# Optimization experiments

Measured on AMD Instinct MI355X. Metric: run time of the kernel, lower is better.

## Reference

```python
import jax, jax.numpy as jnp
import numpy as np

DIM = 1024
NUM_HEADS = 16
HEAD_DIM = DIM // NUM_HEADS
SCALE = HEAD_DIM ** -0.5


def setup_inputs() -> dict:
    key = jax.random.key(0)
    k1, k2, k3 = jax.random.split(key, 3)
    B, S = 2, 2048
    x = jax.random.normal(k1, (B, S, DIM), dtype=jnp.float32)
    # nn.Linear(dim, 3*dim, bias=False): store as [in, out] for x @ W
    w_qkv = jax.random.normal(k2, (DIM, 3 * DIM), dtype=jnp.float32) * (DIM ** -0.5)
    w_out = jax.random.normal(k3, (DIM, DIM), dtype=jnp.float32) * (DIM ** -0.5)
    return {"x": x, "w_qkv": w_qkv, "w_out": w_out}


def reference(x, w_qkv, w_out):
    B, S, _ = x.shape
    qkv = x @ w_qkv                               # [B,S,3*D]
    q, k, v = jnp.split(qkv, 3, axis=-1)          # each [B,S,D]
    def heads(t):
        return t.reshape(B, S, NUM_HEADS, HEAD_DIM).transpose(0, 2, 1, 3)  # [B,H,S,d]
    q, k, v = heads(q), heads(k), heads(v)
    scores = jnp.einsum('bhqd,bhkd->bhqk', q, k) * SCALE   # [B,H,S,S]
    probs = jax.nn.softmax(scores, axis=-1)
    out = jnp.einsum('bhqk,bhkd->bhqd', probs, v)          # [B,H,S,d]
    out = out.transpose(0, 2, 1, 3).reshape(B, S, DIM)
    return out @ w_out
```

## Files before the change

kernel.cpp:

```cpp
#include <hip/hip_runtime.h>


typedef __bf16 bf16x8 __attribute__((ext_vector_type(8)));
typedef __bf16 bf16x4 __attribute__((ext_vector_type(4)));
typedef float floatx4 __attribute__((ext_vector_type(4)));

#define MFMA16(a, b, c) __builtin_amdgcn_mfma_f32_16x16x32_bf16((a), (b), (c), 0, 0, 0)

__device__ __forceinline__ void gl_lds16(const void* g, void* l) {
  __builtin_amdgcn_global_load_lds((__attribute__((address_space(1))) void*)(g),
                                   (__attribute__((address_space(3))) void*)(l),
                                   16, 0, 0);
}

__global__ __launch_bounds__(256) void cast_x(const float* __restrict__ x,
                                              __bf16* __restrict__ xb) {
  int i = (blockIdx.x * 256 + threadIdx.x) * 4;
  float4 v = *(const float4*)(x + i);
  bf16x4 o = { (__bf16)v.x, (__bf16)v.y, (__bf16)v.z, (__bf16)v.w };
  *(bf16x4*)(xb + i) = o;
}

__global__ __launch_bounds__(256) void transpose_cast(const float* __restrict__ w,
                                                      __bf16* __restrict__ wt,
                                                      int K, int N) {
  __shared__ float tile[64][65];
  int k0 = blockIdx.x * 64, n0 = blockIdx.y * 64;
  int t = threadIdx.x;
  for (int j = 0; j < 16; ++j) {
    int e = j * 256 + t, r = e >> 6, c = e & 63;
    tile[r][c] = w[(size_t)(k0 + r) * N + n0 + c];
  }
  __syncthreads();
  for (int j = 0; j < 16; ++j) {
    int e = j * 256 + t, r = e >> 6, c = e & 63;
    wt[(size_t)(n0 + r) * K + k0 + c] = (__bf16)tile[c][r];
  }
}

template <typename OutT, bool SPLITV>
__global__ __launch_bounds__(256) void gemm_bt(const __bf16* __restrict__ A,
                                               const __bf16* __restrict__ Bt,
                                               OutT* __restrict__ C,
                                               __bf16* __restrict__ vt, int N) {
  constexpr int K = 1024;
  __shared__ __align__(16) __bf16 aS[128 * 32];
  __shared__ __align__(16) __bf16 bS[128 * 32];
  const int t = threadIdx.x;
  const int lane = t & 63, wave = t >> 6;
  const int l15 = lane & 15, quad = lane >> 4;
  const int wm = wave >> 1, wn = wave & 1;
  const int m0 = blockIdx.y * 128, n0 = blockIdx.x * 128;

  const floatx4 fzero = {0.f, 0.f, 0.f, 0.f};
  floatx4 acc[4][4];
  for (int mt = 0; mt < 4; ++mt)
    for (int nt = 0; nt < 4; ++nt) acc[mt][nt] = fzero;

  const int arow = t >> 2;
  const int ach = ((t & 3) ^ (arow & 3)) * 8;
  const __bf16* gA0 = A + (size_t)(m0 + arow) * K + ach;
  const __bf16* gA1 = gA0 + (size_t)64 * K;
  const __bf16* gB0 = Bt + (size_t)(n0 + arow) * K + ach;
  const __bf16* gB1 = gB0 + (size_t)64 * K;
  const int swz = (quad ^ (l15 & 3)) * 8;

  for (int k0 = 0; k0 < K; k0 += 32) {
    __syncthreads();
    gl_lds16(gA0 + k0, (char*)aS + t * 16);
    gl_lds16(gA1 + k0, (char*)aS + 4096 + t * 16);
    gl_lds16(gB0 + k0, (char*)bS + t * 16);
    gl_lds16(gB1 + k0, (char*)bS + 4096 + t * 16);
    __syncthreads();

    bf16x8 af[4], bfr[4];
    for (int mt = 0; mt < 4; ++mt)
      af[mt] = *(const bf16x8*)(aS + (wm * 64 + mt * 16 + l15) * 32 + swz);
    for (int nt = 0; nt < 4; ++nt)
      bfr[nt] = *(const bf16x8*)(bS + (wn * 64 + nt * 16 + l15) * 32 + swz);
    for (int mt = 0; mt < 4; ++mt)
      for (int nt = 0; nt < 4; ++nt)
        acc[mt][nt] = MFMA16(af[mt], bfr[nt], acc[mt][nt]);
  }

  for (int mt = 0; mt < 4; ++mt) {
    int row = m0 + wm * 64 + mt * 16 + quad * 4;
    for (int nt = 0; nt < 4; ++nt) {
      int col0 = n0 + wn * 64 + nt * 16;
      if (SPLITV && col0 >= 2048) {
        int dfull = col0 + l15 - 2048;
        int bh = ((row >> 11) << 4) + (dfull >> 6);
        int d = dfull & 63, s0 = row & 2047;
        bf16x4 pk = { (__bf16)acc[mt][nt][0], (__bf16)acc[mt][nt][1],
                      (__bf16)acc[mt][nt][2], (__bf16)acc[mt][nt][3] };
        *(bf16x4*)(vt + ((size_t)bh * 64 + d) * 2048 + s0) = pk;
      } else {
        int col = col0 + l15;
        OutT* cp = C + (size_t)row * N + col;
        for (int r = 0; r < 4; ++r) cp[(size_t)r * N] = (OutT)acc[mt][nt][r];
      }
    }
  }
}

__global__ __launch_bounds__(256) void flash_attn(const __bf16* __restrict__ qkv,
                                                  const __bf16* __restrict__ vt,
                                                  __bf16* __restrict__ out) {
  constexpr float SCALE = 0.125f;
  __shared__ __align__(16) __bf16 kS[2 * 64 * 64];
  __shared__ __align__(16) __bf16 vS[2 * 64 * 64];
  __shared__ __align__(16) __bf16 pT[64 * 64];

  const int t = threadIdx.x;
  const int lane = t & 63, wave = t >> 6;
  const int l15 = lane & 15, quad = lane >> 4;
  const int qb = blockIdx.x, bh = blockIdx.y;
  const int b = bh >> 4, h = bh & 15;

  bf16x8 qf[2][2];
  for (int qt = 0; qt < 2; ++qt) {
    const __bf16* qp = qkv +
        (size_t)(b * 2048 + qb * 128 + wave * 32 + qt * 16 + l15) * 3072 + h * 64 + quad * 8;
    qf[qt][0] = *(const bf16x8*)qp;
    qf[qt][1] = *(const bf16x8*)(qp + 32);
  }

  const floatx4 fzero = {0.f, 0.f, 0.f, 0.f};
  floatx4 oacc[2][4];
  float lsum[2] = {0.f, 0.f};
  for (int qt = 0; qt < 2; ++qt)
    for (int dt = 0; dt < 4; ++dt) oacc[qt][dt] = fzero;

  const int srow = t >> 3, schk = (t & 7) ^ (srow & 7);
  const __bf16* kg0 =
      qkv + (size_t)(b * 2048 + srow) * 3072 + 1024 + h * 64 + schk * 8;
  const __bf16* kg1 = kg0 + (size_t)32 * 3072;
  const __bf16* vg0 = vt + (size_t)bh * 64 * 2048 + (size_t)srow * 2048 + schk * 8;
  const __bf16* vg1 = vg0 + (size_t)32 * 2048;

  const int l7 = l15 & 7;
  const int prow = wave * 16 + l15;

  gl_lds16(kg0, (char*)kS + t * 16);
  gl_lds16(kg1, (char*)kS + 4096 + t * 16);
  gl_lds16(vg0, (char*)vS + t * 16);
  gl_lds16(vg1, (char*)vS + 4096 + t * 16);

  for (int nb = 0; nb < 32; ++nb) {
    __syncthreads();

    if (nb < 31) {
      const size_t n1 = (size_t)(nb + 1) * 64;
      const int oB = ((nb + 1) & 1) * 8192;
      gl_lds16(kg0 + n1 * 3072, (char*)kS + oB + t * 16);
      gl_lds16(kg1 + n1 * 3072, (char*)kS + oB + 4096 + t * 16);
      gl_lds16(vg0 + n1, (char*)vS + oB + t * 16);
      gl_lds16(vg1 + n1, (char*)vS + oB + 4096 + t * 16);
    }

    const __bf16* kC = kS + (nb & 1) * 4096;
    const __bf16* vC = vS + (nb & 1) * 4096;

    bf16x8 kf[4][2];
    for (int nt = 0; nt < 4; ++nt)
      for (int ks = 0; ks < 2; ++ks)
        kf[nt][ks] = *(const bf16x8*)(kC + (nt * 16 + l15) * 64 +
                                      ((ks * 4 + quad) ^ l7) * 8);
    bf16x8 vf[2][4];
    for (int ks = 0; ks < 2; ++ks)
      for (int dt = 0; dt < 4; ++dt)
        vf[ks][dt] = *(const bf16x8*)(vC + (dt * 16 + l15) * 64 +
                                      ((ks * 4 + quad) ^ l7) * 8);

    for (int qt = 0; qt < 2; ++qt) {
      floatx4 sa[4];
      for (int nt = 0; nt < 4; ++nt) {
        floatx4 a = fzero;
        a = MFMA16(kf[nt][0], qf[qt][0], a);
        a = MFMA16(kf[nt][1], qf[qt][1], a);
        sa[nt] = a;
      }
      float ls = 0.f;
      __bf16* pw = pT + (size_t)prow * 64;
      for (int nt = 0; nt < 4; ++nt) {
        float p0 = __expf(sa[nt][0] * SCALE);
        float p1 = __expf(sa[nt][1] * SCALE);
        float p2 = __expf(sa[nt][2] * SCALE);
        float p3 = __expf(sa[nt][3] * SCALE);
        ls += (p0 + p1) + (p2 + p3);
        bf16x4 pk = { (__bf16)p0, (__bf16)p1, (__bf16)p2, (__bf16)p3 };
        *(bf16x4*)(pw + ((nt * 2 + (quad >> 1)) ^ l7) * 8 + (quad & 1) * 4) = pk;
      }
      lsum[qt] += ls;
      for (int ks = 0; ks < 2; ++ks) {
        bf16x8 pa = *(const bf16x8*)(pw + ((ks * 4 + quad) ^ l7) * 8);
        for (int dt = 0; dt < 4; ++dt)
          oacc[qt][dt] = MFMA16(pa, vf[ks][dt], oacc[qt][dt]);
      }
    }
  }

  for (int qt = 0; qt < 2; ++qt) {
    float ls = lsum[qt];
    ls += __shfl_xor(ls, 16);
    ls += __shfl_xor(ls, 32);
    float inv[4];
    for (int r = 0; r < 4; ++r) inv[r] = 1.f / __shfl(ls, quad * 4 + r);
    __bf16* ob = out +
        (size_t)(b * 2048 + qb * 128 + wave * 32 + qt * 16 + quad * 4) * 1024 + h * 64;
    for (int dt = 0; dt < 4; ++dt)
      for (int r = 0; r < 4; ++r)
        ob[(size_t)r * 1024 + dt * 16 + l15] = (__bf16)(oacc[qt][dt][r] * inv[r]);
  }
}

extern "C" void kernel_launch(void* const* d_in, const int* in_sizes, int n_in,
                              void* d_out, int out_size, void* d_ws, size_t ws_size,
                              hipStream_t stream) {
  const float* x = (const float*)d_in[0];
  const float* w_qkv = (const float*)d_in[1];
  const float* w_out = (const float*)d_in[2];
  float* out = (float*)d_out;

  char* ws = (char*)d_ws;
  __bf16* xb = (__bf16*)(ws);
  __bf16* wqkvt = (__bf16*)(ws + ((size_t)8 << 20));
  __bf16* woutt = (__bf16*)(ws + ((size_t)14 << 20));
  __bf16* qkv = (__bf16*)(ws + ((size_t)16 << 20));
  __bf16* vtg = (__bf16*)(ws + ((size_t)40 << 20));
  __bf16* aout = (__bf16*)(ws + ((size_t)48 << 20));

  cast_x<<<4096, 256, 0, stream>>>(x, xb);
  transpose_cast<<<dim3(16, 48), 256, 0, stream>>>(w_qkv, wqkvt, 1024, 3072);
  transpose_cast<<<dim3(16, 16), 256, 0, stream>>>(w_out, woutt, 1024, 1024);
  gemm_bt<__bf16, true><<<dim3(24, 32), 256, 0, stream>>>(xb, wqkvt, qkv, vtg, 3072);
  flash_attn<<<dim3(16, 32), 256, 0, stream>>>(qkv, vtg, aout);
  gemm_bt<float, false><<<dim3(8, 32), 256, 0, stream>>>(aout, woutt, out, nullptr, 1024);
}
```

Measured before the change: 210.4 us.

## Fuse prep kernels, double query tile per attention block, add narrow-N output GEMM

Merges the x cast and both weight transpose-casts into one prep kernel, removing two launches. Flash attention now covers 256 queries per block (64 per wave), so each K/V tile loaded into LDS serves twice as many queries, at the cost of more registers, launch_bounds(256,1) and half as many blocks (256). The output projection uses a new 128x64-tile GEMM, giving 512 blocks instead of 256 to fill more CUs, with single-buffered K loop and syncs on each step.

```diff
diff --git a/kernel.cpp b/kernel.cpp
--- a/kernel.cpp
+++ b/kernel.cpp
@@ -13,20 +13,31 @@
                                    16, 0, 0);
 }
 
-__global__ __launch_bounds__(256) void cast_x(const float* __restrict__ x,
-                                              __bf16* __restrict__ xb) {
-  int i = (blockIdx.x * 256 + threadIdx.x) * 4;
-  float4 v = *(const float4*)(x + i);
-  bf16x4 o = { (__bf16)v.x, (__bf16)v.y, (__bf16)v.z, (__bf16)v.w };
-  *(bf16x4*)(xb + i) = o;
-}
-
-__global__ __launch_bounds__(256) void transpose_cast(const float* __restrict__ w,
-                                                      __bf16* __restrict__ wt,
-                                                      int K, int N) {
+__global__ __launch_bounds__(256) void prep(const float* __restrict__ x,
+                                            const float* __restrict__ w_qkv,
+                                            const float* __restrict__ w_out,
+                                            __bf16* __restrict__ xb,
+                                            __bf16* __restrict__ wqkvt,
+                                            __bf16* __restrict__ woutt) {
   __shared__ float tile[64][65];
-  int k0 = blockIdx.x * 64, n0 = blockIdx.y * 64;
-  int t = threadIdx.x;
+  const int bid = blockIdx.x, t = threadIdx.x;
+  if (bid < 4096) {
+    int i = (bid * 256 + t) * 4;
+    float4 v = *(const float4*)(x + i);
+    bf16x4 o = { (__bf16)v.x, (__bf16)v.y, (__bf16)v.z, (__bf16)v.w };
+    *(bf16x4*)(xb + i) = o;
+    return;
+  }
+  const float* w;
+  __bf16* wt;
+  int K = 1024, N, k0, n0;
+  if (bid < 4864) {
+    int i = bid - 4096;
+    w = w_qkv; wt = wqkvt; N = 3072; k0 = (i & 15) * 64; n0 = (i >> 4) * 64;
+  } else {
+    int i = bid - 4864;
+    w = w_out; wt = woutt; N = 1024; k0 = (i & 15) * 64; n0 = (i >> 4) * 64;
+  }
   for (int j = 0; j < 16; ++j) {
     int e = j * 256 + t, r = e >> 6, c = e & 63;
     tile[r][c] = w[(size_t)(k0 + r) * N + n0 + c];
@@ -103,13 +114,63 @@
   }
 }
 
-__global__ __launch_bounds__(256) void flash_attn(const __bf16* __restrict__ qkv,
-                                                  const __bf16* __restrict__ vt,
-                                                  __bf16* __restrict__ out) {
+__global__ __launch_bounds__(256) void gemm_n64(const __bf16* __restrict__ A,
+                                                const __bf16* __restrict__ Bt,
+                                                float* __restrict__ C) {
+  constexpr int K = 1024, N = 1024;
+  __shared__ __align__(16) __bf16 aS[128 * 32];
+  __shared__ __align__(16) __bf16 bS[64 * 32];
+  const int t = threadIdx.x;
+  const int lane = t & 63, wave = t >> 6;
+  const int l15 = lane & 15, quad = lane >> 4;
+  const int m0 = blockIdx.y * 128, n0 = blockIdx.x * 64;
+
+  const floatx4 fzero = {0.f, 0.f, 0.f, 0.f};
+  floatx4 acc[2][4];
+  for (int mt = 0; mt < 2; ++mt)
+    for (int nt = 0; nt < 4; ++nt) acc[mt][nt] = fzero;
+
+  const int arow = t >> 2;
+  const int ach = ((t & 3) ^ (arow & 3)) * 8;
+  const __bf16* gA0 = A + (size_t)(m0 + arow) * K + ach;
+  const __bf16* gA1 = gA0 + (size_t)64 * K;
+  const __bf16* gB0 = Bt + (size_t)(n0 + arow) * K + ach;
+  const int swz = (quad ^ (l15 & 3)) * 8;
+
+  for (int k0 = 0; k0 < K; k0 += 32) {
+    __syncthreads();
+    gl_lds16(gA0 + k0, (char*)aS + t * 16);
+    gl_lds16(gA1 + k0, (char*)aS + 4096 + t * 16);
+    gl_lds16(gB0 + k0, (char*)bS + t * 16);
+    __syncthreads();
+
+    bf16x8 af[2], bfr[4];
+    for (int mt = 0; mt < 2; ++mt)
+      af[mt] = *(const bf16x8*)(aS + (wave * 32 + mt * 16 + l15) * 32 + swz);
+    for (int nt = 0; nt < 4; ++nt)
+      bfr[nt] = *(const bf16x8*)(bS + (nt * 16 + l15) * 32 + swz);
+    for (int mt = 0; mt < 2; ++mt)
+      for (int nt = 0; nt < 4; ++nt)
+        acc[mt][nt] = MFMA16(af[mt], bfr[nt], acc[mt][nt]);
+  }
+
+  for (int mt = 0; mt < 2; ++mt) {
+    int row = m0 + wave * 32 + mt * 16 + quad * 4;
+    for (int nt = 0; nt < 4; ++nt) {
+      int col = n0 + nt * 16 + l15;
+      float* cp = C + (size_t)row * N + col;
+      for (int r = 0; r < 4; ++r) cp[(size_t)r * N] = acc[mt][nt][r];
+    }
+  }
+}
+
+__global__ __launch_bounds__(256, 1) void flash_attn(const __bf16* __restrict__ qkv,
+                                                     const __bf16* __restrict__ vt,
+                                                     __bf16* __restrict__ out) {
   constexpr float SCALE = 0.125f;
   __shared__ __align__(16) __bf16 kS[2 * 64 * 64];
   __shared__ __align__(16) __bf16 vS[2 * 64 * 64];
-  __shared__ __align__(16) __bf16 pT[64 * 64];
+  __shared__ __align__(16) __bf16 pT[4 * 16 * 64];
 
   const int t = threadIdx.x;
   const int lane = t & 63, wave = t >> 6;
@@ -117,18 +178,18 @@
   const int qb = blockIdx.x, bh = blockIdx.y;
   const int b = bh >> 4, h = bh & 15;
 
-  bf16x8 qf[2][2];
-  for (int qt = 0; qt < 2; ++qt) {
+  bf16x8 qf[4][2];
+  for (int qt = 0; qt < 4; ++qt) {
     const __bf16* qp = qkv +
-        (size_t)(b * 2048 + qb * 128 + wave * 32 + qt * 16 + l15) * 3072 + h * 64 + quad * 8;
+        (size_t)(b * 2048 + qb * 256 + wave * 64 + qt * 16 + l15) * 3072 + h * 64 + quad * 8;
     qf[qt][0] = *(const bf16x8*)qp;
     qf[qt][1] = *(const bf16x8*)(qp + 32);
   }
 
   const floatx4 fzero = {0.f, 0.f, 0.f, 0.f};
-  floatx4 oacc[2][4];
-  float lsum[2] = {0.f, 0.f};
-  for (int qt = 0; qt < 2; ++qt)
+  floatx4 oacc[4][4];
+  float lsum[4] = {0.f, 0.f, 0.f, 0.f};
+  for (int qt = 0; qt < 4; ++qt)
     for (int dt = 0; dt < 4; ++dt) oacc[qt][dt] = fzero;
 
   const int srow = t >> 3, schk = (t & 7) ^ (srow & 7);
@@ -139,7 +200,7 @@
   const __bf16* vg1 = vg0 + (size_t)32 * 2048;
 
   const int l7 = l15 & 7;
-  const int prow = wave * 16 + l15;
+  __bf16* pw = pT + wave * 1024 + l15 * 64;
 
   gl_lds16(kg0, (char*)kS + t * 16);
   gl_lds16(kg1, (char*)kS + 4096 + t * 16);
@@ -172,7 +233,7 @@
         vf[ks][dt] = *(const bf16x8*)(vC + (dt * 16 + l15) * 64 +
                                       ((ks * 4 + quad) ^ l7) * 8);
 
-    for (int qt = 0; qt < 2; ++qt) {
+    for (int qt = 0; qt < 4; ++qt) {
       floatx4 sa[4];
       for (int nt = 0; nt < 4; ++nt) {
         floatx4 a = fzero;
@@ -181,7 +242,6 @@
         sa[nt] = a;
       }
       float ls = 0.f;
-      __bf16* pw = pT + (size_t)prow * 64;
       for (int nt = 0; nt < 4; ++nt) {
         float p0 = __expf(sa[nt][0] * SCALE);
         float p1 = __expf(sa[nt][1] * SCALE);
@@ -200,14 +260,14 @@
     }
   }
 
-  for (int qt = 0; qt < 2; ++qt) {
+  for (int qt = 0; qt < 4; ++qt) {
     float ls = lsum[qt];
     ls += __shfl_xor(ls, 16);
     ls += __shfl_xor(ls, 32);
     float inv[4];
     for (int r = 0; r < 4; ++r) inv[r] = 1.f / __shfl(ls, quad * 4 + r);
     __bf16* ob = out +
-        (size_t)(b * 2048 + qb * 128 + wave * 32 + qt * 16 + quad * 4) * 1024 + h * 64;
+        (size_t)(b * 2048 + qb * 256 + wave * 64 + qt * 16 + quad * 4) * 1024 + h * 64;
     for (int dt = 0; dt < 4; ++dt)
       for (int r = 0; r < 4; ++r)
         ob[(size_t)r * 1024 + dt * 16 + l15] = (__bf16)(oacc[qt][dt][r] * inv[r]);
@@ -230,10 +290,8 @@
   __bf16* vtg = (__bf16*)(ws + ((size_t)40 << 20));
   __bf16* aout = (__bf16*)(ws + ((size_t)48 << 20));
 
-  cast_x<<<4096, 256, 0, stream>>>(x, xb);
-  transpose_cast<<<dim3(16, 48), 256, 0, stream>>>(w_qkv, wqkvt, 1024, 3072);
-  transpose_cast<<<dim3(16, 16), 256, 0, stream>>>(w_out, woutt, 1024, 1024);
+  prep<<<5120, 256, 0, stream>>>(x, w_qkv, w_out, xb, wqkvt, woutt);
   gemm_bt<__bf16, true><<<dim3(24, 32), 256, 0, stream>>>(xb, wqkvt, qkv, vtg, 3072);
-  flash_attn<<<dim3(16, 32), 256, 0, stream>>>(qkv, vtg, aout);
-  gemm_bt<float, false><<<dim3(8, 32), 256, 0, stream>>>(aout, woutt, out, nullptr, 1024);
-}
+  flash_attn<<<dim3(8, 32), 256, 0, stream>>>(qkv, vtg, aout);
+  gemm_n64<<<dim3(16, 32), 256, 0, stream>>>(aout, woutt, out);
+}
```

New measurement: 213.9 us. No clear change (+1.7%).
